# Kernel optimization log

Measured on AMD Instinct MI355X. Metric: run time of the kernel, lower is better.

The kernel has to match this reference:

```python
import jax, jax.numpy as jnp
import numpy as np

EMBED = 1024
HEADS = 16
HEAD_DIM = EMBED // HEADS


def setup_inputs() -> dict:
    key = jax.random.key(0)
    ks = jax.random.split(key, 7)
    B, S = 4, 2048
    q = jax.random.normal(ks[0], (B, S, EMBED), dtype=jnp.float32)
    k = jax.random.normal(ks[1], (B, S, EMBED), dtype=jnp.float32)
    v = jax.random.normal(ks[2], (B, S, EMBED), dtype=jnp.float32)
    # causal mask, broadcast over heads: [B, 1, S, S]
    mask = jnp.broadcast_to(jnp.tril(jnp.ones((S, S), dtype=jnp.int32))[None, None], (B, 1, S, S))
    scale = 1.0 / np.sqrt(EMBED)
    w_q = jax.random.normal(ks[3], (EMBED, EMBED), dtype=jnp.float32) * scale
    w_k = jax.random.normal(ks[4], (EMBED, EMBED), dtype=jnp.float32) * scale
    w_v = jax.random.normal(ks[5], (EMBED, EMBED), dtype=jnp.float32) * scale
    w_o = jax.random.normal(ks[6], (EMBED, EMBED), dtype=jnp.float32) * scale
    return {"q": q, "k": k, "v": v, "mask": mask,
            "w_q": w_q, "w_k": w_k, "w_v": w_v, "w_o": w_o}


def reference(q, k, v, mask, w_q, w_k, w_v, w_o):
    B, S, _ = q.shape
    # Linear projections (torch Linear: x @ W^T), split into heads: [B,H,S,D]
    def proj(x, w):
        return (x @ w.T).reshape(B, -1, HEADS, HEAD_DIM).transpose(0, 2, 1, 3)
    qh, kh, vh = proj(q, w_q), proj(k, w_k), proj(v, w_v)
    scores = jnp.einsum('bhqd,bhkd->bhqk', qh, kh) / jnp.sqrt(jnp.float32(HEAD_DIM))
    scores = jnp.where(mask == 0, jnp.float32(-1e9), scores)
    attn = jax.nn.softmax(scores, axis=-1)
    # dropout is identity in eval/reference mode
    x = jnp.einsum('bhqk,bhkd->bhqd', attn, vh)  # [B,H,S,D]
    x = x.transpose(0, 2, 1, 3).reshape(B, S, HEADS * HEAD_DIM)
    return x @ w_o.T
```

## Files before the change

### kernel.cpp

```cpp
#include <hip/hip_runtime.h>

typedef unsigned short u16;
typedef __attribute__((ext_vector_type(8))) short v8s;
typedef __attribute__((ext_vector_type(4))) float v4f;

#define S_LEN  2048
#define NHEADS 16
#define DHEAD  64
#define EMB    1024

#if __has_builtin(__builtin_amdgcn_exp2f)
#define EXP2F __builtin_amdgcn_exp2f
#else
#define EXP2F exp2f
#endif

__device__ __forceinline__ u16 f32_bf16(float f) {
  union { float f; unsigned u; } x; x.f = f;
  unsigned r = x.u + 0x7fffu + ((x.u >> 16) & 1u);
  return (u16)(r >> 16);
}

__device__ __forceinline__ void async16(const void* g, void* l) {
  __builtin_amdgcn_global_load_lds(
      (const __attribute__((address_space(1))) unsigned int*)g,
      (__attribute__((address_space(3))) unsigned int*)l, 16, 0, 0);
}

__global__ __launch_bounds__(256) void cvt_all(
    const float4* __restrict__ s0, const float4* __restrict__ s1,
    const float4* __restrict__ s2, const float4* __restrict__ s3,
    const float4* __restrict__ s4, const float4* __restrict__ s5,
    const float4* __restrict__ s6,
    ushort4* __restrict__ d0, ushort4* __restrict__ d1,
    ushort4* __restrict__ d2, ushort4* __restrict__ d3,
    ushort4* __restrict__ d4, ushort4* __restrict__ d5,
    ushort4* __restrict__ d6, int nbig, int nsmall) {
  const int y = blockIdx.y;
  const float4* s; ushort4* d;
  switch (y) {
    case 0: s = s0; d = d0; break;  case 1: s = s1; d = d1; break;
    case 2: s = s2; d = d2; break;  case 3: s = s3; d = d3; break;
    case 4: s = s4; d = d4; break;  case 5: s = s5; d = d5; break;
    default: s = s6; d = d6; break;
  }
  const int n4 = (y < 3) ? nbig : nsmall;
  for (int i = blockIdx.x * 256 + threadIdx.x; i < n4; i += gridDim.x * 256) {
    const float4 v = s[i];
    ushort4 o;
    o.x = f32_bf16(v.x); o.y = f32_bf16(v.y);
    o.z = f32_bf16(v.z); o.w = f32_bf16(v.w);
    d[i] = o;
  }
}

__global__ __launch_bounds__(256) void gemm_qkv(const u16* __restrict__ A,
                                                const u16* __restrict__ W0,
                                                const u16* __restrict__ W1,
                                                const u16* __restrict__ W2,
                                                u16* __restrict__ Cq,
                                                u16* __restrict__ Ck,
                                                u16* __restrict__ Cv) {
  __shared__ __align__(16) u16 lA[128 * 32];
  __shared__ __align__(16) u16 lB[128 * 32];
  const int K = EMB;
  const int t = threadIdx.x;
  const int lane = t & 63, w = t >> 6;
  const int m0 = blockIdx.x << 7, n0 = blockIdx.y << 7;
  const int sec = m0 >> 13;
  const u16* W = (sec == 0) ? W0 : ((sec == 1) ? W1 : W2);
  u16* C = (sec == 0) ? Cq : ((sec == 1) ? Ck : Cv);
  const int wm = (w >> 1) << 6, wn = (w & 1) << 6;
  const int qr = lane >> 4, cl = lane & 15;

  v4f acc[4][4];
#pragma unroll
  for (int i = 0; i < 4; ++i)
#pragma unroll
    for (int j = 0; j < 4; ++j) acc[i][j] = (v4f){0.f, 0.f, 0.f, 0.f};

  for (int kt = 0; kt < (K >> 5); ++kt) {
    const int k0 = kt << 5;
    __syncthreads();
#pragma unroll
    for (int i = 0; i < 2; ++i) {
      const int c = t + (i << 8);
      async16(A + (size_t)(m0 + (c >> 2)) * K + k0 + ((c & 3) << 3),
              &lA[(w * 64 + i * 256) * 8]);
      async16(W + (size_t)(n0 + (c >> 2)) * K + k0 + ((c & 3) << 3),
              &lB[(w * 64 + i * 256) * 8]);
    }
    __syncthreads();
    v8s af[4], bf[4];
#pragma unroll
    for (int mi = 0; mi < 4; ++mi)
      af[mi] = *(const v8s*)&lA[(wm + mi * 16 + cl) * 32 + qr * 8];
#pragma unroll
    for (int ni = 0; ni < 4; ++ni)
      bf[ni] = *(const v8s*)&lB[(wn + ni * 16 + cl) * 32 + qr * 8];
#pragma unroll
    for (int mi = 0; mi < 4; ++mi)
#pragma unroll
      for (int ni = 0; ni < 4; ++ni)
        acc[mi][ni] = __builtin_amdgcn_mfma_f32_16x16x32_bf16(af[mi], bf[ni],
                                                              acc[mi][ni], 0, 0, 0);
  }

#pragma unroll
  for (int mi = 0; mi < 4; ++mi)
#pragma unroll
    for (int ni = 0; ni < 4; ++ni)
#pragma unroll
      for (int r = 0; r < 4; ++r) {
        const int mloc = (m0 & 8191) + wm + mi * 16 + qr * 4 + r;
        const int n = n0 + wn + ni * 16 + cl;
        const int b = mloc >> 11, s = mloc & (S_LEN - 1);
        const int h = n >> 6, d = n & (DHEAD - 1);
        const size_t idx = (sec < 2)
            ? (((size_t)b * NHEADS + h) * S_LEN + s) * DHEAD + d
            : (((size_t)b * NHEADS + h) * DHEAD + d) * S_LEN + s;
        C[idx] = f32_bf16(acc[mi][ni][r]);
      }
}

__global__ __launch_bounds__(256) void gemm_out(const u16* __restrict__ A,
                                                const u16* __restrict__ W,
                                                float* __restrict__ C,
                                                int M, int N, int K) {
  __shared__ __align__(16) u16 lA[128 * 32];
  __shared__ __align__(16) u16 lB[128 * 32];
  const int t = threadIdx.x;
  const int lane = t & 63, w = t >> 6;
  const int m0 = blockIdx.x << 7, n0 = blockIdx.y << 7;
  const int wm = (w >> 1) << 6, wn = (w & 1) << 6;
  const int qr = lane >> 4, cl = lane & 15;

  v4f acc[4][4];
#pragma unroll
  for (int i = 0; i < 4; ++i)
#pragma unroll
    for (int j = 0; j < 4; ++j) acc[i][j] = (v4f){0.f, 0.f, 0.f, 0.f};

  for (int kt = 0; kt < (K >> 5); ++kt) {
    const int k0 = kt << 5;
    __syncthreads();
#pragma unroll
    for (int i = 0; i < 2; ++i) {
      const int c = t + (i << 8);
      async16(A + (size_t)(m0 + (c >> 2)) * K + k0 + ((c & 3) << 3),
              &lA[(w * 64 + i * 256) * 8]);
      async16(W + (size_t)(n0 + (c >> 2)) * K + k0 + ((c & 3) << 3),
              &lB[(w * 64 + i * 256) * 8]);
    }
    __syncthreads();
    v8s af[4], bf[4];
#pragma unroll
    for (int mi = 0; mi < 4; ++mi)
      af[mi] = *(const v8s*)&lA[(wm + mi * 16 + cl) * 32 + qr * 8];
#pragma unroll
    for (int ni = 0; ni < 4; ++ni)
      bf[ni] = *(const v8s*)&lB[(wn + ni * 16 + cl) * 32 + qr * 8];
#pragma unroll
    for (int mi = 0; mi < 4; ++mi)
#pragma unroll
      for (int ni = 0; ni < 4; ++ni)
        acc[mi][ni] = __builtin_amdgcn_mfma_f32_16x16x32_bf16(af[mi], bf[ni],
                                                              acc[mi][ni], 0, 0, 0);
  }

#pragma unroll
  for (int mi = 0; mi < 4; ++mi)
#pragma unroll
    for (int ni = 0; ni < 4; ++ni)
#pragma unroll
      for (int r = 0; r < 4; ++r) {
        const int m = m0 + wm + mi * 16 + qr * 4 + r;
        const int n = n0 + wn + ni * 16 + cl;
        C[(size_t)m * N + n] = acc[mi][ni][r];
      }
}

__global__ __launch_bounds__(256) void attn_causal(const u16* __restrict__ Qp,
                                                   const u16* __restrict__ Kp,
                                                   const u16* __restrict__ VpT,
                                                   u16* __restrict__ Out) {
  __shared__ __align__(16) u16 lK[64 * 64];
  __shared__ __align__(16) u16 lV[64 * 64];
  __shared__ __align__(16) u16 pb[4][32 * 64];
  const int t = threadIdx.x;
  const int lane = t & 63, w = t >> 6;
  const int qr = lane >> 4, cl = lane & 15;
  const int qt = 15 - blockIdx.x;
  const int h = blockIdx.y, b = blockIdx.z;
  const int q0 = qt << 7;
  const size_t bh = ((size_t)b * NHEADS + h) * S_LEN * DHEAD;
  const u16* Qb = Qp + bh;
  const u16* Kb = Kp + bh;
  const u16* Vb = VpT + bh;

  const int wr0 = q0 + w * 32;
  v8s aq[2][2];
#pragma unroll
  for (int mf = 0; mf < 2; ++mf)
#pragma unroll
    for (int kf = 0; kf < 2; ++kf)
      aq[mf][kf] = *(const v8s*)(Qb + (size_t)(wr0 + mf * 16 + cl) * DHEAD +
                                 kf * 32 + qr * 8);

  v4f o[2][4], lac[2];
#pragma unroll
  for (int mf = 0; mf < 2; ++mf) {
    lac[mf] = (v4f){0.f, 0.f, 0.f, 0.f};
#pragma unroll
    for (int nf = 0; nf < 4; ++nf) o[mf][nf] = (v4f){0.f, 0.f, 0.f, 0.f};
  }
  v8s vone;
#pragma unroll
  for (int j = 0; j < 8; ++j) vone[j] = (short)0x3F80;

  const float SC = 0.125f * 1.4426950408889634f;

  const int nkt = 2 * qt + 2;
  for (int kt = 0; kt < nkt; ++kt) {
    const int k0 = kt << 6;
    __syncthreads();
#pragma unroll
    for (int i = 0; i < 2; ++i) {
      const int c = t + (i << 8);
      const int krow = c >> 3, kdc = (c & 7) ^ (krow & 7);
      async16(Kb + (size_t)(k0 + krow) * DHEAD + kdc * 8,
              &lK[(w * 64 + (i << 8)) * 8]);
      const int vd = c >> 3, vkc = (c & 7) ^ (vd & 7);
      async16(Vb + (size_t)vd * S_LEN + k0 + vkc * 8,
              &lV[(w * 64 + (i << 8)) * 8]);
    }
    __syncthreads();
    if (k0 > wr0 + 31) continue;

    v4f sacc[2][4];
#pragma unroll
    for (int mf = 0; mf < 2; ++mf)
#pragma unroll
      for (int ni = 0; ni < 4; ++ni) sacc[mf][ni] = (v4f){0.f, 0.f, 0.f, 0.f};
#pragma unroll
    for (int kf = 0; kf < 2; ++kf)
#pragma unroll
      for (int ni = 0; ni < 4; ++ni) {
        const v8s bk = *(const v8s*)&lK[((ni * 16 + cl) * 8 +
                                         (((kf << 2) + qr) ^ (cl & 7))) * 8];
        sacc[0][ni] = __builtin_amdgcn_mfma_f32_16x16x32_bf16(aq[0][kf], bk,
                                                              sacc[0][ni], 0, 0, 0);
        sacc[1][ni] = __builtin_amdgcn_mfma_f32_16x16x32_bf16(aq[1][kf], bk,
                                                              sacc[1][ni], 0, 0, 0);
      }

#pragma unroll
    for (int mf = 0; mf < 2; ++mf) {
      const int rowb0 = wr0 + mf * 16;
      if (k0 + 63 <= rowb0) {
#pragma unroll
        for (int ni = 0; ni < 4; ++ni) {
          const int kc = ni * 2 + (cl >> 3);
#pragma unroll
          for (int r = 0; r < 4; ++r) {
            const float e = EXP2F(sacc[mf][ni][r] * SC);
            pb[w][((kc * 32 + mf * 16 + r * 4 + qr) << 3) + (cl & 7)] =
                (u16)(__float_as_uint(e) >> 16);
          }
        }
      } else {
        const int rowb = rowb0 + qr * 4;
#pragma unroll
        for (int ni = 0; ni < 4; ++ni) {
          const int col = k0 + ni * 16 + cl;
          const int kc = ni * 2 + (cl >> 3);
#pragma unroll
          for (int r = 0; r < 4; ++r) {
            float e = EXP2F(sacc[mf][ni][r] * SC);
            if (col > rowb + r) e = 0.f;
            pb[w][((kc * 32 + mf * 16 + r * 4 + qr) << 3) + (cl & 7)] =
                (u16)(__float_as_uint(e) >> 16);
          }
        }
      }
    }

#pragma unroll
    for (int kf = 0; kf < 2; ++kf) {
      const int kc = (kf << 2) + qr;
      const int sig0 = ((cl & 3) << 2) + (cl >> 2);
      const v8s ap0 = *(const v8s*)&pb[w][((kc * 32 + sig0) << 3)];
      const v8s ap1 = *(const v8s*)&pb[w][((kc * 32 + 16 + sig0) << 3)];
      lac[0] = __builtin_amdgcn_mfma_f32_16x16x32_bf16(ap0, vone, lac[0], 0, 0, 0);
      lac[1] = __builtin_amdgcn_mfma_f32_16x16x32_bf16(ap1, vone, lac[1], 0, 0, 0);
#pragma unroll
      for (int nf = 0; nf < 4; ++nf) {
        const v8s bv = *(const v8s*)&lV[((nf * 16 + cl) * 8 +
                                         (kc ^ (cl & 7))) * 8];
        o[0][nf] = __builtin_amdgcn_mfma_f32_16x16x32_bf16(ap0, bv, o[0][nf], 0, 0, 0);
        o[1][nf] = __builtin_amdgcn_mfma_f32_16x16x32_bf16(ap1, bv, o[1][nf], 0, 0, 0);
      }
    }
  }

#pragma unroll
  for (int mf = 0; mf < 2; ++mf) {
    float inv[4];
#pragma unroll
    for (int r = 0; r < 4; ++r) inv[r] = 1.0f / lac[mf][r];
#pragma unroll
    for (int nf = 0; nf < 4; ++nf)
#pragma unroll
      for (int r = 0; r < 4; ++r) {
        const int row = wr0 + mf * 16 + qr * 4 + r;
        const int col = h * DHEAD + nf * 16 + cl;
        Out[((size_t)b * S_LEN + row) * EMB + col] = f32_bf16(o[mf][nf][r] * inv[r]);
      }
  }
}

extern "C" void kernel_launch(void* const* d_in, const int* in_sizes, int n_in,
                              void* d_out, int out_size, void* d_ws, size_t ws_size,
                              hipStream_t stream) {
  (void)in_sizes; (void)n_in; (void)out_size; (void)ws_size;
  const float* q  = (const float*)d_in[0];
  const float* k  = (const float*)d_in[1];
  const float* v  = (const float*)d_in[2];
  const float* wq = (const float*)d_in[4];
  const float* wk = (const float*)d_in[5];
  const float* wv = (const float*)d_in[6];
  const float* wo = (const float*)d_in[7];
  float* out = (float*)d_out;

  const size_t MT = (size_t)4 * S_LEN * EMB;
  const size_t WT = (size_t)EMB * EMB;
  u16* p = (u16*)d_ws;
  u16* xq = p; p += MT;
  u16* xk = p; p += MT;
  u16* xv = p; p += MT;
  u16* wqb = p; p += WT;
  u16* wkb = p; p += WT;
  u16* wvb = p; p += WT;
  u16* wob = p; p += WT;
  u16* Qp = p; p += MT;
  u16* Kp = p; p += MT;
  u16* Vp = p; p += MT;
  u16* Ao = xq;

  const dim3 blk(256);
  hipLaunchKernelGGL(cvt_all, dim3(512, 7), blk, 0, stream,
                     (const float4*)q, (const float4*)k, (const float4*)v,
                     (const float4*)wq, (const float4*)wk, (const float4*)wv,
                     (const float4*)wo,
                     (ushort4*)xq, (ushort4*)xk, (ushort4*)xv,
                     (ushort4*)wqb, (ushort4*)wkb, (ushort4*)wvb, (ushort4*)wob,
                     (int)(MT / 4), (int)(WT / 4));
  hipLaunchKernelGGL(gemm_qkv, dim3(192, 8), blk, 0, stream,
                     xq, wqb, wkb, wvb, Qp, Kp, Vp);
  hipLaunchKernelGGL(attn_causal, dim3(16, NHEADS, 4), blk, 0, stream, Qp, Kp, Vp, Ao);
  hipLaunchKernelGGL(gemm_out, dim3(64, 8), blk, 0, stream, Ao, wob, out,
                     8192, 1024, 1024);
}
```

Measured before the change: 407.8 us.

## Double-buffer K/V tiles in causal attention and remap grid to a 1D order

The attention kernel now keeps two K/V buffers in shared memory. It issues the async loads for the next 64-key tile before computing on the current one, which drops the second barrier per iteration so loads can overlap the MFMA work. The 3D grid becomes a 1D grid. Block IDs are remapped so groups of 8 head/batch columns are walked from the heaviest query tiles down, aiming at better load balance and cache locality. The change doubles K/V shared-memory use and relies on the async loads for the current buffer having finished by the single barrier, which could race if those loads are not waited on.

```diff
diff --git a/kernel.cpp b/kernel.cpp
--- a/kernel.cpp
+++ b/kernel.cpp
@@ -184,14 +184,16 @@
                                                    const u16* __restrict__ Kp,
                                                    const u16* __restrict__ VpT,
                                                    u16* __restrict__ Out) {
-  __shared__ __align__(16) u16 lK[64 * 64];
-  __shared__ __align__(16) u16 lV[64 * 64];
+  __shared__ __align__(16) u16 lK[2][64 * 64];
+  __shared__ __align__(16) u16 lV[2][64 * 64];
   __shared__ __align__(16) u16 pb[4][32 * 64];
   const int t = threadIdx.x;
   const int lane = t & 63, w = t >> 6;
   const int qr = lane >> 4, cl = lane & 15;
-  const int qt = 15 - blockIdx.x;
-  const int h = blockIdx.y, b = blockIdx.z;
+  const int id = blockIdx.x;
+  const int col = (id & 7) + (((id >> 3) >> 4) << 3);
+  const int qt = 15 - ((id >> 3) & 15);
+  const int h = col & 15, b = col >> 4;
   const int q0 = qt << 7;
   const size_t bh = ((size_t)b * NHEADS + h) * S_LEN * DHEAD;
   const u16* Qb = Qp + bh;
@@ -219,22 +221,34 @@
   for (int j = 0; j < 8; ++j) vone[j] = (short)0x3F80;
 
   const float SC = 0.125f * 1.4426950408889634f;
-
   const int nkt = 2 * qt + 2;
+
+#pragma unroll
+  for (int i = 0; i < 2; ++i) {
+    const int c = t + (i << 8);
+    const int krow = c >> 3, kdc = (c & 7) ^ (krow & 7);
+    async16(Kb + (size_t)krow * DHEAD + kdc * 8, &lK[0][(w * 64 + (i << 8)) * 8]);
+    const int vd = c >> 3, vkc = (c & 7) ^ (vd & 7);
+    async16(Vb + (size_t)vd * S_LEN + vkc * 8, &lV[0][(w * 64 + (i << 8)) * 8]);
+  }
+
   for (int kt = 0; kt < nkt; ++kt) {
     const int k0 = kt << 6;
-    __syncthreads();
-#pragma unroll
-    for (int i = 0; i < 2; ++i) {
-      const int c = t + (i << 8);
-      const int krow = c >> 3, kdc = (c & 7) ^ (krow & 7);
-      async16(Kb + (size_t)(k0 + krow) * DHEAD + kdc * 8,
-              &lK[(w * 64 + (i << 8)) * 8]);
-      const int vd = c >> 3, vkc = (c & 7) ^ (vd & 7);
-      async16(Vb + (size_t)vd * S_LEN + k0 + vkc * 8,
-              &lV[(w * 64 + (i << 8)) * 8]);
-    }
-    __syncthreads();
+    const int cb = kt & 1;
+    __syncthreads();
+    if (kt + 1 < nkt) {
+      const int kn = (kt + 1) << 6;
+#pragma unroll
+      for (int i = 0; i < 2; ++i) {
+        const int c = t + (i << 8);
+        const int krow = c >> 3, kdc = (c & 7) ^ (krow & 7);
+        async16(Kb + (size_t)(kn + krow) * DHEAD + kdc * 8,
+                &lK[1 - cb][(w * 64 + (i << 8)) * 8]);
+        const int vd = c >> 3, vkc = (c & 7) ^ (vd & 7);
+        async16(Vb + (size_t)vd * S_LEN + kn + vkc * 8,
+                &lV[1 - cb][(w * 64 + (i << 8)) * 8]);
+      }
+    }
     if (k0 > wr0 + 31) continue;
 
     v4f sacc[2][4];
@@ -246,8 +260,8 @@
     for (int kf = 0; kf < 2; ++kf)
 #pragma unroll
       for (int ni = 0; ni < 4; ++ni) {
-        const v8s bk = *(const v8s*)&lK[((ni * 16 + cl) * 8 +
-                                         (((kf << 2) + qr) ^ (cl & 7))) * 8];
+        const v8s bk = *(const v8s*)&lK[cb][((ni * 16 + cl) * 8 +
+                                            (((kf << 2) + qr) ^ (cl & 7))) * 8];
         sacc[0][ni] = __builtin_amdgcn_mfma_f32_16x16x32_bf16(aq[0][kf], bk,
                                                               sacc[0][ni], 0, 0, 0);
         sacc[1][ni] = __builtin_amdgcn_mfma_f32_16x16x32_bf16(aq[1][kf], bk,
@@ -272,12 +286,12 @@
         const int rowb = rowb0 + qr * 4;
 #pragma unroll
         for (int ni = 0; ni < 4; ++ni) {
-          const int col = k0 + ni * 16 + cl;
+          const int colk = k0 + ni * 16 + cl;
           const int kc = ni * 2 + (cl >> 3);
 #pragma unroll
           for (int r = 0; r < 4; ++r) {
             float e = EXP2F(sacc[mf][ni][r] * SC);
-            if (col > rowb + r) e = 0.f;
+            if (colk > rowb + r) e = 0.f;
             pb[w][((kc * 32 + mf * 16 + r * 4 + qr) << 3) + (cl & 7)] =
                 (u16)(__float_as_uint(e) >> 16);
           }
@@ -295,8 +309,8 @@
       lac[1] = __builtin_amdgcn_mfma_f32_16x16x32_bf16(ap1, vone, lac[1], 0, 0, 0);
 #pragma unroll
       for (int nf = 0; nf < 4; ++nf) {
-        const v8s bv = *(const v8s*)&lV[((nf * 16 + cl) * 8 +
-                                         (kc ^ (cl & 7))) * 8];
+        const v8s bv = *(const v8s*)&lV[cb][((nf * 16 + cl) * 8 +
+                                            (kc ^ (cl & 7))) * 8];
         o[0][nf] = __builtin_amdgcn_mfma_f32_16x16x32_bf16(ap0, bv, o[0][nf], 0, 0, 0);
         o[1][nf] = __builtin_amdgcn_mfma_f32_16x16x32_bf16(ap1, bv, o[1][nf], 0, 0, 0);
       }
@@ -313,8 +327,8 @@
 #pragma unroll
       for (int r = 0; r < 4; ++r) {
         const int row = wr0 + mf * 16 + qr * 4 + r;
-        const int col = h * DHEAD + nf * 16 + cl;
-        Out[((size_t)b * S_LEN + row) * EMB + col] = f32_bf16(o[mf][nf][r] * inv[r]);
+        const int colo = h * DHEAD + nf * 16 + cl;
+        Out[((size_t)b * S_LEN + row) * EMB + colo] = f32_bf16(o[mf][nf][r] * inv[r]);
       }
   }
 }
@@ -357,7 +371,7 @@
                      (int)(MT / 4), (int)(WT / 4));
   hipLaunchKernelGGL(gemm_qkv, dim3(192, 8), blk, 0, stream,
                      xq, wqb, wkb, wvb, Qp, Kp, Vp);
-  hipLaunchKernelGGL(attn_causal, dim3(16, NHEADS, 4), blk, 0, stream, Qp, Kp, Vp, Ao);
+  hipLaunchKernelGGL(attn_causal, dim3(1024), blk, 0, stream, Qp, Kp, Vp, Ao);
   hipLaunchKernelGGL(gemm_out, dim3(64, 8), blk, 0, stream, Ao, wob, out,
                      8192, 1024, 1024);
 }
```

New measurement: 388.5 us. 1.05x faster.
